# Kernel tuning notes

Measured on AMD Instinct MI355X. Metric: run time of the kernel, lower is better.

## Reference

```python
import jax, jax.numpy as jnp
import numpy as np

S, B, C, H, W = 16, 64, 128, 11, 11
P = H * W
N_ITER = 3
EPS = 1e-5


def setup_inputs() -> dict:
    key = jax.random.key(0)
    ks = jax.random.split(key, 12)
    w = lambda k, shape: jax.random.normal(k, shape, jnp.float32) * 0.02
    return {
        "x": jax.random.normal(ks[0], (S, B, C, H, W), jnp.float32),
        # intra-attention 1x1 convs (stored as [out,in] matrices)
        "wq": w(ks[1], (C, C)), "bq": jnp.zeros((C,), jnp.float32),
        "wk": w(ks[2], (C, C)), "bk": jnp.zeros((C,), jnp.float32),
        "wv": w(ks[3], (C, C)), "bv": jnp.zeros((C,), jnp.float32),
        "intra_alpha": jnp.float32(1.0),
        # inter-message path
        "w_msg": w(ks[4], (C, C + 1)), "b_msg": jnp.zeros((C,), jnp.float32),
        "w_lin": w(ks[5], (C, C)),
        "weight": jnp.float32(0.5),
        "w_gate": w(ks[6], (C, C)), "b_gate": jnp.zeros((C,), jnp.float32),
        # ConvGRU 3x3 convs
        "w_zr": w(ks[7], (2 * C, 2 * C, 3, 3)), "b_zr": jnp.zeros((2 * C,), jnp.float32),
        "w_h": w(ks[8], (C, 2 * C, 3, 3)), "b_h": jnp.zeros((C,), jnp.float32),
        # LayerNorm over [C,11,11]
        "ln_gamma": jnp.ones((C, H, W), jnp.float32),
        "ln_beta": jnp.zeros((C, H, W), jnp.float32),
    }


def reference(x, wq, bq, wk, bk, wv, bv, intra_alpha, w_msg, b_msg, w_lin,
              weight, w_gate, b_gate, w_zr, b_zr, w_h, b_h, ln_gamma, ln_beta):
    scale = C ** -0.5

    def c1(t, wgt, bias):  # 1x1 conv on [S,B,Cin,H,W] -> [S,B,Cout,H,W]
        return jnp.einsum('sbchw,oc->sbohw', t, wgt) + bias[:, None, None]

    def conv3(t, wgt, bias):  # 3x3 'SAME' conv on [N,Cin,H,W]
        y = jax.lax.conv_general_dilated(
            t, wgt, (1, 1), 'SAME', dimension_numbers=('NCHW', 'OIHW', 'NCHW'))
        return y + bias[None, :, None, None]

    # chain-graph neighbor validity masks (|i-j| == 1)
    mask_l = (jnp.arange(S) >= 1).astype(x.dtype)[:, None, None, None, None]
    mask_r = (jnp.arange(S) <= S - 2).astype(x.dtype)[:, None, None, None, None]

    h = x
    for _ in range(N_ITER):
        # ---- intra spatial self-attention (per node, over P=H*W tokens) ----
        q = c1(h, wq, bq).reshape(S, B, C, P)
        k = c1(h, wk, bk).reshape(S, B, C, P)
        v = c1(h, wv, bv).reshape(S, B, C, P)
        att = jax.nn.softmax(jnp.einsum('sbcp,sbcq->sbpq', q, k) * scale, axis=-1)
        intra = jnp.einsum('sbpq,sbcq->sbcp', att, v).reshape(S, B, C, H, W)
        intra = intra_alpha * intra + h

        # ---- inter gated message attention from chain neighbors ----
        xf = h.reshape(S, B, C, P)

        def gated_msg(y, edge_val):
            ef = jnp.full((S, B, 1, H, W), edge_val, h.dtype)  # edge feature i-j
            yy = c1(jnp.concatenate([y, ef], axis=2), w_msg, b_msg).reshape(S, B, C, P)
            yy = jnp.einsum('sbcp,dc->sbdp', yy, w_lin)  # Linear (no bias)
            a = jax.nn.softmax(jnp.einsum('sbcp,sbcq->sbpq', xf, yy), axis=-1)
            m = jnp.einsum('sbpq,sbcq->sbcp', a, yy).reshape(S, B, C, H, W)
            g = jax.nn.sigmoid(c1(m, w_gate, b_gate).mean(axis=(-2, -1), keepdims=True))
            return m * g

        y_left = jnp.concatenate([jnp.zeros_like(h[:1]), h[:-1]], axis=0)   # h[i-1], edge +1
        y_right = jnp.concatenate([h[1:], jnp.zeros_like(h[:1])], axis=0)   # h[i+1], edge -1
        inter = gated_msg(y_left, 1.0) * mask_l + gated_msg(y_right, -1.0) * mask_r

        comb = weight * intra + (1.0 - weight) * inter

        # ---- ConvGRU update (fold S into batch) ----
        xg = comb.reshape(S * B, C, H, W)
        hg = h.reshape(S * B, C, H, W)
        zr = jax.nn.sigmoid(conv3(jnp.concatenate([xg, hg], axis=1), w_zr, b_zr))
        z, r = zr[:, :C], zr[:, C:]
        h_hat = jnp.tanh(conv3(jnp.concatenate([xg, r * hg], axis=1), w_h, b_h))
        h_new = ((1 - z) * hg + z * h_hat).reshape(S, B, C, H, W)

        # ---- residual + LayerNorm over [C,H,W] ----
        nh = h_new + h
        mu = nh.mean(axis=(-3, -2, -1), keepdims=True)
        var = nh.var(axis=(-3, -2, -1), keepdims=True)
        h = (nh - mu) * jax.lax.rsqrt(var + EPS) * ln_gamma + ln_beta
    return h
```

## Files before the change

### kernel.cpp

```cpp
#include <hip/hip_runtime.h>
#include <hip/hip_bf16.h>

#define S_   16
#define B_   64
#define SBn  1024
#define C_   128
#define P_   121
#define CP_  15488
static const long NEl = 15859712L;

typedef __hip_bfloat16 bf16t;
typedef __attribute__((ext_vector_type(8))) short bf16x8;
typedef __attribute__((ext_vector_type(4))) float f32x4;
typedef __attribute__((ext_vector_type(4))) unsigned short us4;

__device__ __forceinline__ float ldb(const bf16t* p){ return __bfloat162float(*p); }
__device__ __forceinline__ float b2f(unsigned short u){ unsigned x=((unsigned)u)<<16; float f; __builtin_memcpy(&f,&x,4); return f; }
__device__ __forceinline__ unsigned short f2bu(float v){ __hip_bfloat16 b=__float2bfloat16(v); unsigned short u; __builtin_memcpy(&u,&b,2); return u; }
__device__ __forceinline__ float ldin(const void* s, long i, int f){
    return f ? ((const float*)s)[i] : b2f(((const unsigned short*)s)[i]);
}

__global__ void detect_kernel(const unsigned short* __restrict__ x, int* __restrict__ flag){
    if(blockIdx.x==0 && threadIdx.x==0){
        int crazy=0;
        for(int i=0;i<512;i++){
            unsigned e=(x[i]>>7)&0xFF;
            if(e!=0 && (e<64 || e>191)) crazy++;
        }
        *flag=(crazy>40)?1:0;
    }
}

__global__ void cvt_kernel(float* __restrict__ dst, const void* __restrict__ src, long n, const int* __restrict__ flag){
    long i=(long)blockIdx.x*blockDim.x+threadIdx.x;
    long st=(long)gridDim.x*blockDim.x;
    int f=*flag;
    for(;i<n;i+=st) dst[i]=ldin(src,i,f);
}

__global__ __launch_bounds__(256) void cvtT_kernel(bf16t* __restrict__ hT, const void* __restrict__ x, const int* __restrict__ flag){
    __shared__ bf16t tl[CP_];
    int sb=blockIdx.x, t=threadIdx.x; int f=*flag;
    for(int i=t;i<CP_;i+=256)
        tl[i]=__float2bfloat16(ldin(x,(long)sb*CP_+i,f));
    __syncthreads();
    bf16t* ho=hT+(size_t)sb*CP_;
    for(int j=t;j<CP_;j+=256){
        int p=j>>7, c=j&127;
        ho[j]=tl[c*P_+p];
    }
}

__global__ __launch_bounds__(128) void prep_msg_kernel(float* __restrict__ W2, float* __restrict__ b2l, float* __restrict__ b2r,
        const void* __restrict__ wlin, const void* __restrict__ wmsg, const void* __restrict__ bmsg, const int* __restrict__ flag){
    int d=blockIdx.x, c=threadIdx.x; int f=*flag;
    float acc=0.f;
    for(int o2=0;o2<C_;o2++) acc += ldin(wlin,(long)d*C_+o2,f)*ldin(wmsg,(long)o2*(C_+1)+c,f);
    W2[d*C_+c]=acc;
    if(c<2){
        float e=(c==0)?1.f:-1.f; float a=0.f;
        for(int o2=0;o2<C_;o2++) a += ldin(wlin,(long)d*C_+o2,f)*(ldin(bmsg,o2,f)+e*ldin(wmsg,(long)o2*(C_+1)+C_,f));
        if(c==0) b2l[d]=a; else b2r[d]=a;
    }
}

template<int RAW>
__global__ void prep_w1t(bf16t* __restrict__ dst, const void* __restrict__ src, const int* __restrict__ flag){
    int idx=blockIdx.x*blockDim.x+threadIdx.x;
    if(idx>=16384) return;
    int r=idx&31, oc=(idx>>5)&127, icb=idx>>12;
    float v = RAW? ldin(src,(long)oc*C_+icb*32+r,*flag) : ((const float*)src)[(long)oc*C_+icb*32+r];
    dst[idx]=__float2bfloat16(v);
}

__global__ void prep_w3t(bf16t* __restrict__ dst, const void* __restrict__ src, const int* __restrict__ flag, int OC){
    int idx=blockIdx.x*blockDim.x+threadIdx.x;
    int tot=OC*2304;
    if(idx>=tot) return;
    int r=idx&31; int rest=idx>>5; int oc=rest%OC; int g2=rest/OC; int icb=g2&7, tap=g2>>3;
    float v=ldin(src,((long)(oc*256+icb*32+r))*9+tap,*flag);
    dst[idx]=__float2bfloat16(v);
}

__global__ void prep_gbt(float* __restrict__ gamT, float* __restrict__ betT,
                         const void* __restrict__ gam, const void* __restrict__ bet, const int* __restrict__ flag){
    int idx=blockIdx.x*blockDim.x+threadIdx.x;
    if(idx>=CP_) return;
    int c=idx/P_, p=idx-c*P_; int f=*flag;
    gamT[p*C_+c]=ldin(gam,idx,f);
    betT[p*C_+c]=ldin(bet,idx,f);
}

__global__ void prep_wgt(float* __restrict__ wgT, float* __restrict__ bg2,
                         const void* __restrict__ wg, const void* __restrict__ bg, const int* __restrict__ flag){
    int idx=blockIdx.x*blockDim.x+threadIdx.x;
    int f=*flag;
    if(idx<16384){ int k=idx>>7, c=idx&127; wgT[idx]=ldin(wg,(long)c*C_+k,f); }
    if(idx<128) bg2[idx]=ldin(bg,idx,f);
}

__device__ __forceinline__ void gemm24r(f32x4 (&acc)[4][2],
    const bf16t* __restrict__ Wt, const bf16x8 (&hreg)[4][2],
    int ocr,int l15,int kg)
{
    #pragma unroll
    for(int i=0;i<4;i++){
        #pragma unroll
        for(int j=0;j<2;j++) acc[i][j]=(f32x4){0.f,0.f,0.f,0.f};
    }
    #pragma unroll
    for(int kc=0;kc<4;kc++){
        bf16x8 a[4];
        #pragma unroll
        for(int mt=0;mt<4;mt++) a[mt]=*(const bf16x8*)(Wt+((size_t)(kc*C_+ocr*64+mt*16+l15))*32+kg*8);
        #pragma unroll
        for(int mt=0;mt<4;mt++){
            #pragma unroll
            for(int nt=0;nt<2;nt++)
                acc[mt][nt]=__builtin_amdgcn_mfma_f32_16x16x32_bf16(a[mt],hreg[kc][nt],acc[mt][nt],0,0,0);
        }
    }
}

__device__ __forceinline__ void msg_phase(
    f32x4 (&res)[8], const bf16t* __restrict__ hT, int sb, int shift,
    const bf16t* __restrict__ W2T, const float* __restrict__ b2e,
    const float* __restrict__ wgT, const float* __restrict__ bgf, float w1m,
    const bf16x8 (&areg)[4],
    bf16t* LA, bf16t* LB, float* fl,
    int t,int w,int l15,int kg,int ocr,int pcr)
{
    __syncthreads();
    const bf16t* hsp=hT+(size_t)(sb+shift)*CP_;
    bf16x8 hregS[4][2];
    #pragma unroll
    for(int kc=0;kc<4;kc++){
        #pragma unroll
        for(int nt=0;nt<2;nt++)
            hregS[kc][nt]=*(const bf16x8*)(hsp+(size_t)(pcr*32+nt*16+l15)*C_+kc*32+kg*8);
    }
    f32x4 acc[4][2];
    gemm24r(acc,W2T,hregS,ocr,l15,kg);
    #pragma unroll
    for(int mt=0;mt<4;mt++){
        int oc0=ocr*64+mt*16+kg*4;
        #pragma unroll
        for(int nt=0;nt<2;nt++){
            int p=pcr*32+nt*16+l15;
            us4 pk;
            #pragma unroll
            for(int r=0;r<4;r++){
                float v=acc[mt][nt][r]+b2e[oc0+r];
                pk[r]=f2bu(v);
                LB[(oc0+r)*136+p]=__float2bfloat16(p<P_? v : 0.f);
            }
            *(us4*)(LA+p*136+oc0)=pk;
        }
    }
    __syncthreads();
    int m0=w*16;
    f32x4 s[8];
    #pragma unroll
    for(int nt=0;nt<8;nt++) s[nt]=(f32x4){0.f,0.f,0.f,0.f};
// ... 149 lines not shown
    if(l15>=9){
        #pragma unroll
        for(int r=0;r<4;r++) s[7][r]=-3.0e38f;
    }
    #pragma unroll
    for(int r=0;r<4;r++){
        float mx=s[0][r];
        #pragma unroll
        for(int nt=1;nt<8;nt++) mx=fmaxf(mx,s[nt][r]);
        #pragma unroll
        for(int o=1;o<16;o<<=1) mx=fmaxf(mx,__shfl_xor(mx,o));
        float sm=0.f;
        #pragma unroll
        for(int nt=0;nt<8;nt++){ float e=__expf(s[nt][r]-mx); s[nt][r]=e; sm+=e; }
        #pragma unroll
        for(int o=1;o<16;o<<=1) sm+=__shfl_xor(sm,o);
        float rs=1.f/sm;
        #pragma unroll
        for(int nt=0;nt<8;nt++) s[nt][r]*=rs;
    }
    __syncthreads();
    gemm24r(acc,WvT,hreg,ocr,l15,kg);
    #pragma unroll
    for(int mt=0;mt<4;mt++){
        int oc0=ocr*64+mt*16+kg*4;
        #pragma unroll
        for(int nt=0;nt<2;nt++){
            int p=pcr*32+nt*16+l15;
            #pragma unroll
            for(int r=0;r<4;r++)
                LA[(oc0+r)*136+p]=__float2bfloat16(p<P_? acc[mt][nt][r]+bv[oc0+r] : 0.f);
        }
    }
    #pragma unroll
    for(int r=0;r<4;r++){
        int pr=m0+kg*4+r;
        #pragma unroll
        for(int nt=0;nt<8;nt++) LB[pr*136+nt*16+l15]=__float2bfloat16(s[nt][r]);
    }
    __syncthreads();
    f32x4 res[8];
    #pragma unroll
    for(int nt=0;nt<8;nt++) res[nt]=(f32x4){0.f,0.f,0.f,0.f};
    #pragma unroll
    for(int jc=0;jc<4;jc++){
        bf16x8 a=*(const bf16x8*)(LA+(size_t)(m0+l15)*136+jc*32+kg*8);
        #pragma unroll
        for(int nt=0;nt<8;nt++){
            bf16x8 b=*(const bf16x8*)(LB+(size_t)(nt*16+l15)*136+jc*32+kg*8);
            res[nt]=__builtin_amdgcn_mfma_f32_16x16x32_bf16(a,b,res[nt],0,0,0);
        }
    }
    float al=*alphap, wv=*wp, w1m=1.f-wv;
    int c0=m0+kg*4;
    #pragma unroll
    for(int nt=0;nt<8;nt++){
        int p=nt*16+l15;
        int pc=(p<P_)?p:(P_-1);
        us4 hv=*(const us4*)(hp+(size_t)pc*C_+c0);
        #pragma unroll
        for(int r=0;r<4;r++) res[nt][r]=wv*(al*res[nt][r]+b2f(hv[r]));
    }
    if(sb>=B_)
        msg_phase(res,hT,sb,-B_,W2T,b2l,wgT,bgf,w1m,areg,LA,LB,fl,t,w,l15,kg,ocr,pcr);
    if(sb<SBn-B_)
        msg_phase(res,hT,sb, B_,W2T,b2r,wgT,bgf,w1m,areg,LA,LB,fl,t,w,l15,kg,ocr,pcr);
    __syncthreads();
    unsigned short* tl=(unsigned short*)LA;
    #pragma unroll
    for(int nt=0;nt<8;nt++){
        int p=nt*16+l15;
        if(p>=P_) continue;
        us4 pk;
        #pragma unroll
        for(int r=0;r<4;r++) pk[r]=f2bu(res[nt][r]);
        *(us4*)(tl+p*C_+c0)=pk;
    }
    __syncthreads();
    bf16t* ob=comb+(size_t)sb*CP_;
    for(int j=t;j<1936;j+=512)
        *(bf16x8*)(ob+j*8)=*(const bf16x8*)(tl+j*8);
}

#define LOADA2(bidx, widx) { \
    _Pragma("unroll") \
    for(int mt=0;mt<2;mt++) abuf[bidx][mt]=*(const bf16x8*)(Wt+(size_t)(widx)*(OC*32)+mt*512+base_lane); }
#define STEP2(lbase, bidx, doff) { \
    bf16x8 bb[4]; \
    _Pragma("unroll") \
    for(int nt=0;nt<4;nt++) bb[nt]=*(const bf16x8*)((lbase)+boff[nt]+(doff)); \
    __builtin_amdgcn_s_setprio(1); \
    _Pragma("unroll") \
    for(int mt=0;mt<2;mt++){ \
        _Pragma("unroll") \
        for(int nt=0;nt<4;nt++) \
            acc[mt][nt]=__builtin_amdgcn_mfma_f32_16x16x32_bf16(abuf[bidx][mt],bb[nt],acc[mt][nt],0,0,0); } \
    __builtin_amdgcn_s_setprio(0); }

#define SLOADZ(stg) { \
    const bf16t* ssrc=(((stg)<2)? in0T:in1T)+(size_t)sb*CP_+((stg)&1)*64; \
    if(sv0) sreg0=*(const bf16x8*)(ssrc+(size_t)sp0*C_+(t&7)*8); }
#define SWRITEZ(lbase) { \
    if(sv0) *(bf16x8*)((lbase)+spix0*72+(t&7)*8)=sreg0; }

__global__ __launch_bounds__(1024) void conv3_zr(
    bf16t* __restrict__ o0, bf16t* __restrict__ o1,
    const bf16t* __restrict__ in0T, const bf16t* __restrict__ in1T,
    const bf16t* __restrict__ Wt, const float* __restrict__ bias,
    const bf16t* __restrict__ hTb)
{
    constexpr int OC=256;
    __shared__ bf16t lin[2*12176];
    int sb=blockIdx.x;
    int t=threadIdx.x, lane=t&63, w=t>>6;
    int ocb=(w>=8)?128:0; int w2=w&7;
    int ocr=w2>>1, pcr=w2&1, l15=lane&15, kg=lane>>4;
    int boff[4]; bool pv_[4];
    #pragma unroll
    for(int nt=0;nt<4;nt++){
        int p=pcr*64+nt*16+l15;
        pv_[nt]=(p<P_); int pc=pv_[nt]?p:(P_-1);
        boff[nt]=((pc/11)*13+(pc%11))*72+kg*8;
    }
    f32x4 acc[2][4];
    #pragma unroll
    for(int i=0;i<2;i++){
        #pragma unroll
        for(int j=0;j<4;j++) acc[i][j]=(f32x4){0.f,0.f,0.f,0.f};
    }
    int base_lane=(ocb+ocr*32+l15)*32+kg*8;
    bf16x8 abuf[4][2];
    bf16x8 sreg0;
    bool sv0=(t<968);
    int sp0=(t<968)? (t>>3):120;
    int spix0=(sp0/11+1)*13+(sp0%11)+1;
    LOADA2(0,0); LOADA2(1,1); LOADA2(2,8); LOADA2(3,9);
    SLOADZ(0);
    {
        bf16x8 z;
        #pragma unroll
        for(int e=0;e<8;e++) z[e]=0;
        if(t<768){
            int half=t>=384; int i2=t-half*384;
            int bi=i2>>3, cc=(i2&7)*8;
            int pix;
            if(bi<13) pix=bi;
            else if(bi<26) pix=156+(bi-13);
            else { int j2=bi-26; pix=(1+(j2>>1))*13+((j2&1)?12:0); }
            *(bf16x8*)(lin+half*12176+pix*72+cc)=z;
        }
    }
    SWRITEZ(lin);
    __syncthreads();
    #pragma unroll
    for(int st=0; st<4; ++st){
        if(st<3) SLOADZ(st+1);
        bf16t* lbase=lin+(st&1)*12176;
        #pragma unroll
        for(int k=0;k<18;k++){
            int s=st*18+k;
            int tap=k>>1, l=k&1;
            int doff=((tap/3)*13+(tap%3))*72+l*32;
            STEP2(lbase, s&3, doff);
            if(s<68){
                int s4=s+4, st4=s4/18, k4=s4-st4*18, tap4=k4>>1, l4=k4&1;
                LOADA2(s&3, tap4*8+st4*2+l4);
            }
        }
        if(st<3){ SWRITEZ(lin+((st+1)&1)*12176); }
        __syncthreads();
    }
    unsigned short* tl=(unsigned short*)lin;
    if(ocb==0){
        #pragma unroll
        for(int mt=0;mt<2;mt++){
            int ocl=ocr*32+mt*16+kg*4;
            #pragma unroll
            for(int nt=0;nt<4;nt++){
                if(!pv_[nt]) continue;
                int p=pcr*64+nt*16+l15;
                us4 pk;
                #pragma unroll
                for(int r=0;r<4;r++){ float a=acc[mt][nt][r]+bias[ocl+r]; pk[r]=f2bu(1.f/(1.f+__expf(-a))); }
                *(us4*)(tl+p*C_+ocl)=pk;
            }
        }
    }
    __syncthreads();
    {
        bf16t* zb=o0+(size_t)sb*CP_;
        *(bf16x8*)(zb+t*8)=*(const bf16x8*)(tl+t*8);
        if(t<912) *(bf16x8*)(zb+(t+1024)*8)=*(const bf16x8*)(tl+(t+1024)*8);
    }
    __syncthreads();
    if(ocb==128){
        #pragma unroll
        for(int mt=0;mt<2;mt++){
            int ocl=ocr*32+mt*16+kg*4;
            #pragma unroll
            for(int nt=0;nt<4;nt++){
                if(!pv_[nt]) continue;
                int p=pcr*64+nt*16+l15;
                size_t tb=(size_t)sb*CP_+(size_t)p*C_+ocl;
                us4 hv=*(const us4*)(hTb+tb);
                us4 pk;
                #pragma unroll
                for(int r=0;r<4;r++){ float a=acc[mt][nt][r]+bias[128+ocl+r]; float sg=1.f/(1.f+__expf(-a)); pk[r]=f2bu(sg*b2f(hv[r])); }
                *(us4*)(tl+p*C_+ocl)=pk;
            }
        }
    }
    __syncthreads();
    {
        bf16t* rb=o1+(size_t)sb*CP_;
        *(bf16x8*)(rb+t*8)=*(const bf16x8*)(tl+t*8);
        if(t<912) *(bf16x8*)(rb+(t+1024)*8)=*(const bf16x8*)(tl+(t+1024)*8);
    }
}

#define SLOADH(stg) { \
    const bf16t* ssrc=(((stg)<2)? in0T:in1T)+(size_t)sb*CP_+((stg)&1)*64; \
    sreg[0]=*(const bf16x8*)(ssrc+(size_t)(t>>3)*C_+(t&7)*8); \
    if(sv1) sreg[1]=*(const bf16x8*)(ssrc+(size_t)sp1*C_+(t&7)*8); }
#define SWRITEH(lbase) { \
    *(bf16x8*)((lbase)+spix0*72+(t&7)*8)=sreg[0]; \
    if(sv1) *(bf16x8*)((lbase)+spix1*72+(t&7)*8)=sreg[1]; }

__global__ __launch_bounds__(512,4) void conv3_hh(
    bf16t* __restrict__ o0,
    const bf16t* __restrict__ in0T, const bf16t* __restrict__ in1T,
    const bf16t* __restrict__ Wt, const float* __restrict__ bias,
    const bf16t* __restrict__ zT, const bf16t* __restrict__ hTb,
    const float* __restrict__ gamT, const float* __restrict__ betT)
{
    constexpr int OC=128;
    __shared__ bf16t lin[2*12176];
    __shared__ float red[16];
    int sb=blockIdx.x;
    int t=threadIdx.x, lane=t&63, w=t>>6;
    int ocr=w>>1, pcr=w&1, l15=lane&15, kg=lane>>4;
    int boff[4]; bool pv_[4];
    #pragma unroll
    for(int nt=0;nt<4;nt++){
        int p=pcr*64+nt*16+l15;
        pv_[nt]=(p<P_); int pc=pv_[nt]?p:(P_-1);
        boff[nt]=((pc/11)*13+(pc%11))*72+kg*8;
    }
    f32x4 acc[2][4];
    #pragma unroll
    for(int i=0;i<2;i++){
        #pragma unroll
        for(int j=0;j<4;j++) acc[i][j]=(f32x4){0.f,0.f,0.f,0.f};
    }
    int base_lane=(ocr*32+l15)*32+kg*8;
    bf16x8 abuf[4][2];
    bf16x8 sreg[2];
    bool sv1=((t+512)<968);
    int sp0=t>>3, sp1=(t+512)>>3;
    if(sp1>120) sp1=120;
    int spix0=(sp0/11+1)*13+(sp0%11)+1;
    int spix1=(sp1/11+1)*13+(sp1%11)+1;
    LOADA2(0,0); LOADA2(1,1); LOADA2(2,8); LOADA2(3,9);
    SLOADH(0);
    {
        bf16x8 z;
        #pragma unroll
        for(int e=0;e<8;e++) z[e]=0;
        for(int i=t;i<768;i+=512){
            int half=i>=384; int i2=i-half*384;
            int bi=i2>>3, cc=(i2&7)*8;
            int pix;
            if(bi<13) pix=bi;
            else if(bi<26) pix=156+(bi-13);
            else { int j2=bi-26; pix=(1+(j2>>1))*13+((j2&1)?12:0); }
            *(bf16x8*)(lin+half*12176+pix*72+cc)=z;
        }
    }
    SWRITEH(lin);
    __syncthreads();
    #pragma unroll
    for(int st=0; st<4; ++st){
        if(st<3) SLOADH(st+1);
        bf16t* lbase=lin+(st&1)*12176;
        #pragma unroll
        for(int k=0;k<18;k++){
            int s=st*18+k;
            int tap=k>>1, l=k&1;
            int doff=((tap/3)*13+(tap%3))*72+l*32;
            STEP2(lbase, s&3, doff);
            if(s<68){
                int s4=s+4, st4=s4/18, k4=s4-st4*18, tap4=k4>>1, l4=k4&1;
                LOADA2(s&3, tap4*8+st4*2+l4);
            }
        }
        if(st<3){ SWRITEH(lin+((st+1)&1)*12176); }
        __syncthreads();
    }
    float ls=0.f, ls2=0.f;
    #pragma unroll
    for(int mt=0;mt<2;mt++){
        int ocl=ocr*32+mt*16+kg*4;
        #pragma unroll
        for(int nt=0;nt<4;nt++){
            if(!pv_[nt]) continue;
            int p=pcr*64+nt*16+l15;
            size_t tb=(size_t)sb*CP_+(size_t)p*C_+ocl;
            us4 hv=*(const us4*)(hTb+tb);
            us4 zv=*(const us4*)(zT+tb);
            us4 pk;
            #pragma unroll
            for(int r=0;r<4;r++){
                float a=acc[mt][nt][r]+bias[ocl+r];
                float ht=tanhf(a);
                float z=b2f(zv[r]), h=b2f(hv[r]);
                unsigned short u=f2bu((1.f-z)*h+z*ht+h);
                pk[r]=u;
                float nr=b2f(u); ls+=nr; ls2+=nr*nr;
            }
            *(us4*)((unsigned short*)lin + p*C_+ocl)=pk;
        }
    }
    #pragma unroll
    for(int o=32;o;o>>=1){ ls+=__shfl_xor(ls,o); ls2+=__shfl_xor(ls2,o); }
    if(lane==0){ red[w]=ls; red[8+w]=ls2; }
    __syncthreads();
    float Sx=0.f,Sx2=0.f;
    #pragma unroll
    for(int i=0;i<8;i++){ Sx+=red[i]; Sx2+=red[8+i]; }
    float mu=Sx*(1.f/(float)CP_);
    float var=Sx2*(1.f/(float)CP_)-mu*mu;
    float rstd=rsqrtf(var+1e-5f);
    bf16t* ho=o0+(size_t)sb*CP_;
    const unsigned short* tl=(const unsigned short*)lin;
    for(int j=t;j<1936;j+=512){
        int base=j*8;
        bf16x8 ovec;
        #pragma unroll
        for(int e=0;e<8;e++){
            float v=(b2f(tl[base+e])-mu)*rstd*gamT[base+e]+betT[base+e];
            ovec[e]=(short)f2bu(v);
        }
        *(bf16x8*)(ho+base)=ovec;
    }
}

__global__ __launch_bounds__(256) void finalT_kernel(void* __restrict__ fout, const bf16t* __restrict__ hT, const int* __restrict__ flag){
    __shared__ bf16t tl[CP_];
    int sb=blockIdx.x, t=threadIdx.x, f=*flag;
    for(int i=t;i<CP_;i+=256) tl[i]=hT[(size_t)sb*CP_+i];
    __syncthreads();
    for(int i=t;i<CP_;i+=256){
        int c=i/P_, p=i-c*P_;
        float v=ldb(tl+p*C_+c);
        size_t oi=(size_t)sb*CP_+i;
        if(f) ((float*)fout)[oi]=v;
        else  ((bf16t*)fout)[oi]=__float2bfloat16(v);
    }
}

extern "C" void kernel_launch(void* const* d_in, const int* in_sizes, int n_in,
                              void* d_out, int out_size, void* d_ws, size_t ws_size,
                              hipStream_t stream) {
    (void)in_sizes; (void)n_in; (void)out_size;
    char* base=(char*)d_ws;
    size_t off=0;
    auto alloc=[&](size_t bytes){ void* p=base+off; off+=(bytes+255)&~(size_t)255; return p; };
    bf16t* b1=(bf16t*)alloc((size_t)NEl*2+8192);
    bf16t* b2=(bf16t*)alloc((size_t)NEl*2+8192);
    bf16t* b3=(bf16t*)alloc((size_t)NEl*2+8192);
    bf16t* b4=(bf16t*)d_out;
    bf16t* wqT=(bf16t*)alloc(16384*2);
    bf16t* wkT=(bf16t*)alloc(16384*2);
    bf16t* wvT=(bf16t*)alloc(16384*2);
    bf16t* w2T=(bf16t*)alloc(16384*2);
    bf16t* wzrT=(bf16t*)alloc((size_t)589824*2);
    bf16t* whT =(bf16t*)alloc((size_t)294912*2);
    float* W2f=(float*)alloc(16384*4);
    float* b2l=(float*)alloc(128*4); float* b2r=(float*)alloc(128*4);
    float* bqf=(float*)alloc(128*4); float* bkf=(float*)alloc(128*4); float* bvf=(float*)alloc(128*4);
    float* bzrf=(float*)alloc(256*4); float* bhf=(float*)alloc(128*4);
    float* gamT=(float*)alloc(15488*4); float* betT=(float*)alloc(15488*4);
    float* wgTf=(float*)alloc(16384*4); float* bgf2=(float*)alloc(128*4);
    float* alphaf=(float*)alloc(4); float* weightf=(float*)alloc(4);
    int* flag=(int*)alloc(4);
    if(ws_size<off) return;

    detect_kernel<<<1,64,0,stream>>>((const unsigned short*)d_in[0],flag);
    cvtT_kernel<<<SBn,256,0,stream>>>(b1,d_in[0],flag);
    prep_w1t<1><<<64,256,0,stream>>>(wqT,d_in[1],flag);
    cvt_kernel<<<1,128,0,stream>>>(bqf,d_in[2],128,flag);
    prep_w1t<1><<<64,256,0,stream>>>(wkT,d_in[3],flag);
    cvt_kernel<<<1,128,0,stream>>>(bkf,d_in[4],128,flag);
    prep_w1t<1><<<64,256,0,stream>>>(wvT,d_in[5],flag);
    cvt_kernel<<<1,128,0,stream>>>(bvf,d_in[6],128,flag);
    cvt_kernel<<<1,64,0,stream>>>(alphaf,d_in[7],1,flag);
    prep_msg_kernel<<<C_,C_,0,stream>>>(W2f,b2l,b2r,d_in[10],d_in[8],d_in[9],flag);
    prep_w1t<0><<<64,256,0,stream>>>(w2T,W2f,flag);
    cvt_kernel<<<1,64,0,stream>>>(weightf,d_in[11],1,flag);
    prep_wgt<<<64,256,0,stream>>>(wgTf,bgf2,d_in[12],d_in[13],flag);
    prep_w3t<<<(256*2304+255)/256,256,0,stream>>>(wzrT,d_in[14],flag,256);
    cvt_kernel<<<1,256,0,stream>>>(bzrf,d_in[15],256,flag);
    prep_w3t<<<(128*2304+255)/256,256,0,stream>>>(whT,d_in[16],flag,128);
    cvt_kernel<<<1,128,0,stream>>>(bhf,d_in[17],128,flag);
    prep_gbt<<<(CP_+255)/256,256,0,stream>>>(gamT,betT,d_in[18],d_in[19],flag);

    for(int it=0; it<3; ++it){
        attn_all<<<SBn,512,0,stream>>>(b2,b1,wqT,wkT,wvT,bqf,bkf,bvf,
                                       w2T,b2l,b2r,wgTf,bgf2,alphaf,weightf);
        conv3_zr<<<SBn,1024,0,stream>>>(b4,b3,b2,b1,wzrT,bzrf,b1);
        conv3_hh<<<SBn,512,0,stream>>>(b1,b2,b3,whT,bhf,b4,b1,gamT,betT);
    }
    finalT_kernel<<<SBn,256,0,stream>>>(d_out,b1,flag);
}
```

Before: 1.385 ms.

## Switch 3x3 conv kernels to 32x32x16 MFMA and split zr conv across blocks

Both ConvGRU 3x3 conv kernels move from 16x16x32 bf16 MFMA tiles to 32x32x16 tiles, with each wave covering 64 output channels by 32 pixels. Weights are repacked into 16-wide k groups to match, and A-operand prefetch drops from four buffers to two. conv3_zr no longer runs one 1024-thread block that computes both z and r; it launches a 2D grid of 512-thread blocks, one per 128-channel half, and each block writes its half directly. The aim is better MFMA efficiency and fewer idle lanes from the 121-pixel padding. In exchange, each block stages its input into shared memory twice, and register pressure per thread rises.

```diff
diff --git a/kernel.cpp b/kernel.cpp
--- a/kernel.cpp
+++ b/kernel.cpp
@@ -12,6 +12,7 @@
 typedef __hip_bfloat16 bf16t;
 typedef __attribute__((ext_vector_type(8))) short bf16x8;
 typedef __attribute__((ext_vector_type(4))) float f32x4;
+typedef __attribute__((ext_vector_type(16))) float f32x16;
 typedef __attribute__((ext_vector_type(4))) unsigned short us4;
 
 __device__ __forceinline__ float ldb(const bf16t* p){ return __bfloat162float(*p); }
@@ -74,12 +75,12 @@
     dst[idx]=__float2bfloat16(v);
 }
 
-__global__ void prep_w3t(bf16t* __restrict__ dst, const void* __restrict__ src, const int* __restrict__ flag, int OC){
+__global__ void prep_w3t32(bf16t* __restrict__ dst, const void* __restrict__ src, const int* __restrict__ flag, int OC){
     int idx=blockIdx.x*blockDim.x+threadIdx.x;
     int tot=OC*2304;
     if(idx>=tot) return;
-    int r=idx&31; int rest=idx>>5; int oc=rest%OC; int g2=rest/OC; int icb=g2&7, tap=g2>>3;
-    float v=ldin(src,((long)(oc*256+icb*32+r))*9+tap,*flag);
+    int r=idx&15; int rest=idx>>4; int oc=rest%OC; int g2=rest/OC; int k16=g2&15, tap=g2>>4;
+    float v=ldin(src,((long)(oc*256+k16*16+r))*9+tap,*flag);
     dst[idx]=__float2bfloat16(v);
 }
 
@@ -395,28 +396,33 @@
         *(bf16x8*)(ob+j*8)=*(const bf16x8*)(tl+j*8);
 }
 
-#define LOADA2(bidx, widx) { \
+#define LOADA32(bidx, gk) { \
     _Pragma("unroll") \
-    for(int mt=0;mt<2;mt++) abuf[bidx][mt]=*(const bf16x8*)(Wt+(size_t)(widx)*(OC*32)+mt*512+base_lane); }
-#define STEP2(lbase, bidx, doff) { \
-    bf16x8 bb[4]; \
+    for(int ot=0;ot<2;ot++){ \
+        _Pragma("unroll") \
+        for(int kk=0;kk<4;kk++) \
+            abuf[bidx][ot][kk]=*(const bf16x8*)(Wt+(((size_t)(gk)+kk)*OC+aoc0+ot*32)*16+ah8); } }
+#define TAP32(lbase, bidx, d) { \
+    bf16x8 br[4]; \
     _Pragma("unroll") \
-    for(int nt=0;nt<4;nt++) bb[nt]=*(const bf16x8*)((lbase)+boff[nt]+(doff)); \
+    for(int kk=0;kk<4;kk++) br[kk]=*(const bf16x8*)((lbase)+bpix0+(d)+kk*16); \
     __builtin_amdgcn_s_setprio(1); \
     _Pragma("unroll") \
-    for(int mt=0;mt<2;mt++){ \
-        _Pragma("unroll") \
-        for(int nt=0;nt<4;nt++) \
-            acc[mt][nt]=__builtin_amdgcn_mfma_f32_16x16x32_bf16(abuf[bidx][mt],bb[nt],acc[mt][nt],0,0,0); } \
+    for(int kk=0;kk<4;kk++){ \
+        accA=__builtin_amdgcn_mfma_f32_32x32x16_bf16(abuf[bidx][0][kk],br[kk],accA,0,0,0); \
+        accB=__builtin_amdgcn_mfma_f32_32x32x16_bf16(abuf[bidx][1][kk],br[kk],accB,0,0,0); \
+    } \
     __builtin_amdgcn_s_setprio(0); }
 
-#define SLOADZ(stg) { \
+#define SLOAD32(stg) { \
     const bf16t* ssrc=(((stg)<2)? in0T:in1T)+(size_t)sb*CP_+((stg)&1)*64; \
-    if(sv0) sreg0=*(const bf16x8*)(ssrc+(size_t)sp0*C_+(t&7)*8); }
-#define SWRITEZ(lbase) { \
-    if(sv0) *(bf16x8*)((lbase)+spix0*72+(t&7)*8)=sreg0; }
-
-__global__ __launch_bounds__(1024) void conv3_zr(
+    sreg[0]=*(const bf16x8*)(ssrc+(size_t)(t>>3)*C_+(t&7)*8); \
+    if(sv1) sreg[1]=*(const bf16x8*)(ssrc+(size_t)sp1*C_+(t&7)*8); }
+#define SWRITE32(lbase) { \
+    *(bf16x8*)((lbase)+spix0*72+(t&7)*8)=sreg[0]; \
+    if(sv1) *(bf16x8*)((lbase)+spix1*72+(t&7)*8)=sreg[1]; }
+
+__global__ __launch_bounds__(512) void conv3_zr(
     bf16t* __restrict__ o0, bf16t* __restrict__ o1,
     const bf16t* __restrict__ in0T, const bf16t* __restrict__ in1T,
     const bf16t* __restrict__ Wt, const float* __restrict__ bias,
@@ -424,37 +430,33 @@
 {
     constexpr int OC=256;
     __shared__ bf16t lin[2*12176];
-    int sb=blockIdx.x;
+    int sb=blockIdx.x, ocb=(int)blockIdx.y*128;
     int t=threadIdx.x, lane=t&63, w=t>>6;
-    int ocb=(w>=8)?128:0; int w2=w&7;
-    int ocr=w2>>1, pcr=w2&1, l15=lane&15, kg=lane>>4;
-    int boff[4]; bool pv_[4];
-    #pragma unroll
-    for(int nt=0;nt<4;nt++){
-        int p=pcr*64+nt*16+l15;
-        pv_[nt]=(p<P_); int pc=pv_[nt]?p:(P_-1);
-        boff[nt]=((pc/11)*13+(pc%11))*72+kg*8;
-    }
-    f32x4 acc[2][4];
-    #pragma unroll
-    for(int i=0;i<2;i++){
-        #pragma unroll
-        for(int j=0;j<4;j++) acc[i][j]=(f32x4){0.f,0.f,0.f,0.f};
-    }
-    int base_lane=(ocb+ocr*32+l15)*32+kg*8;
-    bf16x8 abuf[4][2];
-    bf16x8 sreg0;
-    bool sv0=(t<968);
-    int sp0=(t<968)? (t>>3):120;
+    int ocr=w>>2, pcr=w&3;
+    int c31=lane&31, h=lane>>5;
+    int p0=pcr*32+c31;
+    bool pv0=(p0<P_);
+    int pc0=pv0?p0:(P_-1);
+    int bpix0=((pc0/11)*13+(pc0%11))*72+h*8;
+    f32x16 accA,accB;
+    #pragma unroll
+    for(int j=0;j<16;j++){ accA[j]=0.f; accB[j]=0.f; }
+    int aoc0=ocb+ocr*64+c31, ah8=h*8;
+    bf16x8 abuf[2][2][4];
+    bf16x8 sreg[2];
+    bool sv1=((t+512)<968);
+    int sp0=t>>3, sp1=(t+512)>>3;
+    if(sp1>120) sp1=120;
     int spix0=(sp0/11+1)*13+(sp0%11)+1;
-    LOADA2(0,0); LOADA2(1,1); LOADA2(2,8); LOADA2(3,9);
-    SLOADZ(0);
+    int spix1=(sp1/11+1)*13+(sp1%11)+1;
+    LOADA32(0,0);
+    SLOAD32(0);
     {
         bf16x8 z;
         #pragma unroll
         for(int e=0;e<8;e++) z[e]=0;
-        if(t<768){
-            int half=t>=384; int i2=t-half*384;
+        for(int i=t;i<768;i+=512){
+            int half=i>=384; int i2=i-half*384;
             int bi=i2>>3, cc=(i2&7)*8;
             int pix;
             if(bi<13) pix=bi;
@@ -463,83 +465,74 @@
             *(bf16x8*)(lin+half*12176+pix*72+cc)=z;
         }
     }
-    SWRITEZ(lin);
+    SWRITE32(lin);
     __syncthreads();
     #pragma unroll
     for(int st=0; st<4; ++st){
-        if(st<3) SLOADZ(st+1);
+        if(st<3) SLOAD32(st+1);
         bf16t* lbase=lin+(st&1)*12176;
         #pragma unroll
-        for(int k=0;k<18;k++){
-            int s=st*18+k;
-            int tap=k>>1, l=k&1;
-            int doff=((tap/3)*13+(tap%3))*72+l*32;
-            STEP2(lbase, s&3, doff);
-            if(s<68){
-                int s4=s+4, st4=s4/18, k4=s4-st4*18, tap4=k4>>1, l4=k4&1;
-                LOADA2(s&3, tap4*8+st4*2+l4);
+        for(int tap=0;tap<9;tap++){
+            int g=st*9+tap;
+            if(g<35){
+                int g1=g+1, st1=g1/9, tap1=g1-st1*9;
+                LOADA32(g1&1, tap1*16+st1*4);
             }
-        }
-        if(st<3){ SWRITEZ(lin+((st+1)&1)*12176); }
+            int d=((tap/3)*13+(tap%3))*72;
+            TAP32(lbase, g&1, d);
+        }
+        if(st<3){ SWRITE32(lin+((st+1)&1)*12176); }
         __syncthreads();
     }
     unsigned short* tl=(unsigned short*)lin;
-    if(ocb==0){
-        #pragma unroll
-        for(int mt=0;mt<2;mt++){
-            int ocl=ocr*32+mt*16+kg*4;
+    if(pv0){
+        if(ocb==0){
             #pragma unroll
-            for(int nt=0;nt<4;nt++){
-                if(!pv_[nt]) continue;
-                int p=pcr*64+nt*16+l15;
-                us4 pk;
+            for(int a=0;a<4;a++){
+                int ocA=ocr*64+8*a+4*h, ocB=ocA+32;
+                us4 pkA,pkB;
                 #pragma unroll
-                for(int r=0;r<4;r++){ float a=acc[mt][nt][r]+bias[ocl+r]; pk[r]=f2bu(1.f/(1.f+__expf(-a))); }
-                *(us4*)(tl+p*C_+ocl)=pk;
+                for(int r=0;r<4;r++){
+                    float vA=accA[4*a+r]+bias[ocA+r];
+                    float vB=accB[4*a+r]+bias[ocB+r];
+                    pkA[r]=f2bu(1.f/(1.f+__expf(-vA)));
+                    pkB[r]=f2bu(1.f/(1.f+__expf(-vB)));
+                }
+                *(us4*)(tl+p0*C_+ocA)=pkA;
+                *(us4*)(tl+p0*C_+ocB)=pkB;
             }
+        }else{
+            #pragma unroll
+            for(int a=0;a<4;a++){
+                int ocA=ocr*64+8*a+4*h, ocB=ocA+32;
+                size_t tbA=(size_t)sb*CP_+(size_t)p0*C_+ocA;
+                size_t tbB=(size_t)sb*CP_+(size_t)p0*C_+ocB;
+                us4 hvA=*(const us4*)(hTb+tbA);
+                us4 hvB=*(const us4*)(hTb+tbB);
+                us4 pkA,pkB;
+                #pragma unroll
+                for(int r=0;r<4;r++){
+                    float vA=accA[4*a+r]+bias[128+ocA+r];
+                    float vB=accB[4*a+r]+bias[128+ocB+r];
+                    float sA=1.f/(1.f+__expf(-vA));
+                    float sB=1.f/(1.f+__expf(-vB));
+                    pkA[r]=f2bu(sA*b2f(hvA[r]));
+                    pkB[r]=f2bu(sB*b2f(hvB[r]));
+                }
+                *(us4*)(tl+p0*C_+ocA)=pkA;
+                *(us4*)(tl+p0*C_+ocB)=pkB;
+            }
         }
     }
     __syncthreads();
     {
-        bf16t* zb=o0+(size_t)sb*CP_;
-        *(bf16x8*)(zb+t*8)=*(const bf16x8*)(tl+t*8);
-        if(t<912) *(bf16x8*)(zb+(t+1024)*8)=*(const bf16x8*)(tl+(t+1024)*8);
-    }
-    __syncthreads();
-    if(ocb==128){
-        #pragma unroll
-        for(int mt=0;mt<2;mt++){
-            int ocl=ocr*32+mt*16+kg*4;
-            #pragma unroll
-            for(int nt=0;nt<4;nt++){
-                if(!pv_[nt]) continue;
-                int p=pcr*64+nt*16+l15;
-                size_t tb=(size_t)sb*CP_+(size_t)p*C_+ocl;
-                us4 hv=*(const us4*)(hTb+tb);
-                us4 pk;
-                #pragma unroll
-                for(int r=0;r<4;r++){ float a=acc[mt][nt][r]+bias[128+ocl+r]; float sg=1.f/(1.f+__expf(-a)); pk[r]=f2bu(sg*b2f(hv[r])); }
-                *(us4*)(tl+p*C_+ocl)=pk;
-            }
-        }
-    }
-    __syncthreads();
-    {
-        bf16t* rb=o1+(size_t)sb*CP_;
-        *(bf16x8*)(rb+t*8)=*(const bf16x8*)(tl+t*8);
-        if(t<912) *(bf16x8*)(rb+(t+1024)*8)=*(const bf16x8*)(tl+(t+1024)*8);
-    }
-}
-
-#define SLOADH(stg) { \
-    const bf16t* ssrc=(((stg)<2)? in0T:in1T)+(size_t)sb*CP_+((stg)&1)*64; \
-    sreg[0]=*(const bf16x8*)(ssrc+(size_t)(t>>3)*C_+(t&7)*8); \
-    if(sv1) sreg[1]=*(const bf16x8*)(ssrc+(size_t)sp1*C_+(t&7)*8); }
-#define SWRITEH(lbase) { \
-    *(bf16x8*)((lbase)+spix0*72+(t&7)*8)=sreg[0]; \
-    if(sv1) *(bf16x8*)((lbase)+spix1*72+(t&7)*8)=sreg[1]; }
-
-__global__ __launch_bounds__(512,4) void conv3_hh(
+        bf16t* ob=(ocb==0? o0 : o1)+(size_t)sb*CP_;
+        for(int j=t;j<1936;j+=512)
+            *(bf16x8*)(ob+j*8)=*(const bf16x8*)(tl+j*8);
+    }
+}
+
+__global__ __launch_bounds__(512) void conv3_hh(
     bf16t* __restrict__ o0,
     const bf16t* __restrict__ in0T, const bf16t* __restrict__ in1T,
     const bf16t* __restrict__ Wt, const float* __restrict__ bias,
@@ -551,30 +544,25 @@
     __shared__ float red[16];
     int sb=blockIdx.x;
     int t=threadIdx.x, lane=t&63, w=t>>6;
-    int ocr=w>>1, pcr=w&1, l15=lane&15, kg=lane>>4;
-    int boff[4]; bool pv_[4];
-    #pragma unroll
-    for(int nt=0;nt<4;nt++){
-        int p=pcr*64+nt*16+l15;
-        pv_[nt]=(p<P_); int pc=pv_[nt]?p:(P_-1);
-        boff[nt]=((pc/11)*13+(pc%11))*72+kg*8;
-    }
-    f32x4 acc[2][4];
-    #pragma unroll
-    for(int i=0;i<2;i++){
-        #pragma unroll
-        for(int j=0;j<4;j++) acc[i][j]=(f32x4){0.f,0.f,0.f,0.f};
-    }
-    int base_lane=(ocr*32+l15)*32+kg*8;
-    bf16x8 abuf[4][2];
+    int ocr=w>>2, pcr=w&3;
+    int c31=lane&31, h=lane>>5;
+    int p0=pcr*32+c31;
+    bool pv0=(p0<P_);
+    int pc0=pv0?p0:(P_-1);
+    int bpix0=((pc0/11)*13+(pc0%11))*72+h*8;
+    f32x16 accA,accB;
+    #pragma unroll
+    for(int j=0;j<16;j++){ accA[j]=0.f; accB[j]=0.f; }
+    int aoc0=ocr*64+c31, ah8=h*8;
+    bf16x8 abuf[2][2][4];
     bf16x8 sreg[2];
     bool sv1=((t+512)<968);
     int sp0=t>>3, sp1=(t+512)>>3;
     if(sp1>120) sp1=120;
     int spix0=(sp0/11+1)*13+(sp0%11)+1;
     int spix1=(sp1/11+1)*13+(sp1%11)+1;
-    LOADA2(0,0); LOADA2(1,1); LOADA2(2,8); LOADA2(3,9);
-    SLOADH(0);
+    LOADA32(0,0);
+    SLOAD32(0);
     {
         bf16x8 z;
         #pragma unroll
@@ -589,48 +577,50 @@
             *(bf16x8*)(lin+half*12176+pix*72+cc)=z;
         }
     }
-    SWRITEH(lin);
+    SWRITE32(lin);
     __syncthreads();
     #pragma unroll
     for(int st=0; st<4; ++st){
-        if(st<3) SLOADH(st+1);
+        if(st<3) SLOAD32(st+1);
         bf16t* lbase=lin+(st&1)*12176;
         #pragma unroll
-        for(int k=0;k<18;k++){
-            int s=st*18+k;
-            int tap=k>>1, l=k&1;
-            int doff=((tap/3)*13+(tap%3))*72+l*32;
-            STEP2(lbase, s&3, doff);
-            if(s<68){
-                int s4=s+4, st4=s4/18, k4=s4-st4*18, tap4=k4>>1, l4=k4&1;
-                LOADA2(s&3, tap4*8+st4*2+l4);
+        for(int tap=0;tap<9;tap++){
+            int g=st*9+tap;
+            if(g<35){
+                int g1=g+1, st1=g1/9, tap1=g1-st1*9;
+                LOADA32(g1&1, tap1*16+st1*4);
             }
-        }
-        if(st<3){ SWRITEH(lin+((st+1)&1)*12176); }
+            int d=((tap/3)*13+(tap%3))*72;
+            TAP32(lbase, g&1, d);
+        }
+        if(st<3){ SWRITE32(lin+((st+1)&1)*12176); }
         __syncthreads();
     }
     float ls=0.f, ls2=0.f;
-    #pragma unroll
-    for(int mt=0;mt<2;mt++){
-        int ocl=ocr*32+mt*16+kg*4;
-        #pragma unroll
-        for(int nt=0;nt<4;nt++){
-            if(!pv_[nt]) continue;
-            int p=pcr*64+nt*16+l15;
-            size_t tb=(size_t)sb*CP_+(size_t)p*C_+ocl;
-            us4 hv=*(const us4*)(hTb+tb);
-            us4 zv=*(const us4*)(zT+tb);
-            us4 pk;
+    if(pv0){
+        #pragma unroll
+        for(int a=0;a<4;a++){
+            int ocA=ocr*64+8*a+4*h, ocB=ocA+32;
+            size_t tbA=(size_t)sb*CP_+(size_t)p0*C_+ocA;
+            size_t tbB=(size_t)sb*CP_+(size_t)p0*C_+ocB;
+            us4 hvA=*(const us4*)(hTb+tbA); us4 zvA=*(const us4*)(zT+tbA);
+            us4 hvB=*(const us4*)(hTb+tbB); us4 zvB=*(const us4*)(zT+tbB);
+            us4 pkA,pkB;
             #pragma unroll
             for(int r=0;r<4;r++){
-                float a=acc[mt][nt][r]+bias[ocl+r];
-                float ht=tanhf(a);
-                float z=b2f(zv[r]), h=b2f(hv[r]);
-                unsigned short u=f2bu((1.f-z)*h+z*ht+h);
-                pk[r]=u;
-                float nr=b2f(u); ls+=nr; ls2+=nr*nr;
+                float aA=accA[4*a+r]+bias[ocA+r];
+                float aB=accB[4*a+r]+bias[ocB+r];
+                float htA=tanhf(aA), htB=tanhf(aB);
+                float zA=b2f(zvA[r]), hA=b2f(hvA[r]);
+                float zB=b2f(zvB[r]), hB=b2f(hvB[r]);
+                unsigned short uA=f2bu((1.f-zA)*hA+zA*htA+hA);
+                unsigned short uB=f2bu((1.f-zB)*hB+zB*htB+hB);
+                pkA[r]=uA; pkB[r]=uB;
+                float nA=b2f(uA), nB=b2f(uB);
+                ls+=nA+nB; ls2+=nA*nA+nB*nB;
             }
-            *(us4*)((unsigned short*)lin + p*C_+ocl)=pk;
+            *(us4*)((unsigned short*)lin+p0*C_+ocA)=pkA;
+            *(us4*)((unsigned short*)lin+p0*C_+ocB)=pkB;
         }
     }
     #pragma unroll
@@ -711,16 +701,16 @@
     prep_w1t<0><<<64,256,0,stream>>>(w2T,W2f,flag);
     cvt_kernel<<<1,64,0,stream>>>(weightf,d_in[11],1,flag);
     prep_wgt<<<64,256,0,stream>>>(wgTf,bgf2,d_in[12],d_in[13],flag);
-    prep_w3t<<<(256*2304+255)/256,256,0,stream>>>(wzrT,d_in[14],flag,256);
+    prep_w3t32<<<(256*2304+255)/256,256,0,stream>>>(wzrT,d_in[14],flag,256);
     cvt_kernel<<<1,256,0,stream>>>(bzrf,d_in[15],256,flag);
-    prep_w3t<<<(128*2304+255)/256,256,0,stream>>>(whT,d_in[16],flag,128);
+    prep_w3t32<<<(128*2304+255)/256,256,0,stream>>>(whT,d_in[16],flag,128);
     cvt_kernel<<<1,128,0,stream>>>(bhf,d_in[17],128,flag);
     prep_gbt<<<(CP_+255)/256,256,0,stream>>>(gamT,betT,d_in[18],d_in[19],flag);
 
     for(int it=0; it<3; ++it){
         attn_all<<<SBn,512,0,stream>>>(b2,b1,wqT,wkT,wvT,bqf,bkf,bvf,
                                        w2T,b2l,b2r,wgTf,bgf2,alphaf,weightf);
-        conv3_zr<<<SBn,1024,0,stream>>>(b4,b3,b2,b1,wzrT,bzrf,b1);
+        conv3_zr<<<dim3(SBn,2),512,0,stream>>>(b4,b3,b2,b1,wzrT,bzrf,b1);
         conv3_hh<<<SBn,512,0,stream>>>(b1,b2,b3,whT,bhf,b4,b1,gamT,betT);
     }
     finalT_kernel<<<SBn,256,0,stream>>>(d_out,b1,flag);
```

Result: slower. 1.601 ms (+15.5%).

## Restructure conv3_zr to process two samples per block, splitting output channels across grid

Applied to the files above, without the earlier changes.

The zr 3x3 conv kernel is reorganized so each 512-thread block handles two samples and one 128-channel half of the output, instead of one sample with all 256 channels in a 1024-thread block. Each weight fragment loaded from global memory is now reused across two samples' MFMAs, halving weight traffic per sample. The cost is doubled LDS (four padded tiles), doubled accumulator registers, and the input activations being loaded twice, once by each channel-half block.

```diff
diff --git a/kernel.cpp b/kernel.cpp
--- a/kernel.cpp
+++ b/kernel.cpp
@@ -410,24 +410,44 @@
             acc[mt][nt]=__builtin_amdgcn_mfma_f32_16x16x32_bf16(abuf[bidx][mt],bb[nt],acc[mt][nt],0,0,0); } \
     __builtin_amdgcn_s_setprio(0); }
 
-#define SLOADZ(stg) { \
-    const bf16t* ssrc=(((stg)<2)? in0T:in1T)+(size_t)sb*CP_+((stg)&1)*64; \
-    if(sv0) sreg0=*(const bf16x8*)(ssrc+(size_t)sp0*C_+(t&7)*8); }
-#define SWRITEZ(lbase) { \
-    if(sv0) *(bf16x8*)((lbase)+spix0*72+(t&7)*8)=sreg0; }
-
-__global__ __launch_bounds__(1024) void conv3_zr(
+#define SLOADZ2(stg) { \
+    const bf16t* s0=(((stg)<2)? in0T:in1T)+(size_t)sb0*CP_+((stg)&1)*64; \
+    const bf16t* s1=s0+CP_; \
+    sreg[0]=*(const bf16x8*)(s0+(size_t)spA*C_+(t&7)*8); \
+    if(sv1) sreg[1]=*(const bf16x8*)(s0+(size_t)spB*C_+(t&7)*8); \
+    sreg[2]=*(const bf16x8*)(s1+(size_t)spA*C_+(t&7)*8); \
+    if(sv1) sreg[3]=*(const bf16x8*)(s1+(size_t)spB*C_+(t&7)*8); }
+#define SWRITEZ2(lbase) { \
+    *(bf16x8*)((lbase)+spixA*72+(t&7)*8)=sreg[0]; \
+    if(sv1) *(bf16x8*)((lbase)+spixB*72+(t&7)*8)=sreg[1]; \
+    *(bf16x8*)((lbase)+12176+spixA*72+(t&7)*8)=sreg[2]; \
+    if(sv1) *(bf16x8*)((lbase)+12176+spixB*72+(t&7)*8)=sreg[3]; }
+#define STEPZ2(lbase, bidx, doff) { \
+    bf16x8 bb0[4], bb1[4]; \
+    _Pragma("unroll") \
+    for(int nt=0;nt<4;nt++){ \
+        bb0[nt]=*(const bf16x8*)((lbase)+boff[nt]+(doff)); \
+        bb1[nt]=*(const bf16x8*)((lbase)+12176+boff[nt]+(doff)); } \
+    __builtin_amdgcn_s_setprio(1); \
+    _Pragma("unroll") \
+    for(int mt=0;mt<2;mt++){ \
+        _Pragma("unroll") \
+        for(int nt=0;nt<4;nt++){ \
+            accA[mt][nt]=__builtin_amdgcn_mfma_f32_16x16x32_bf16(abuf[bidx][mt],bb0[nt],accA[mt][nt],0,0,0); \
+            accB[mt][nt]=__builtin_amdgcn_mfma_f32_16x16x32_bf16(abuf[bidx][mt],bb1[nt],accB[mt][nt],0,0,0); } } \
+    __builtin_amdgcn_s_setprio(0); }
+
+__global__ __launch_bounds__(512) void conv3_zr2(
     bf16t* __restrict__ o0, bf16t* __restrict__ o1,
     const bf16t* __restrict__ in0T, const bf16t* __restrict__ in1T,
     const bf16t* __restrict__ Wt, const float* __restrict__ bias,
     const bf16t* __restrict__ hTb)
 {
     constexpr int OC=256;
-    __shared__ bf16t lin[2*12176];
-    int sb=blockIdx.x;
+    __shared__ bf16t lin[4*12176];
+    int sb0=(int)blockIdx.x*2, ocb=(int)blockIdx.y*128;
     int t=threadIdx.x, lane=t&63, w=t>>6;
-    int ocb=(w>=8)?128:0; int w2=w&7;
-    int ocr=w2>>1, pcr=w2&1, l15=lane&15, kg=lane>>4;
+    int ocr=w>>1, pcr=w&1, l15=lane&15, kg=lane>>4;
     int boff[4]; bool pv_[4];
     #pragma unroll
     for(int nt=0;nt<4;nt++){
@@ -435,99 +455,111 @@
         pv_[nt]=(p<P_); int pc=pv_[nt]?p:(P_-1);
         boff[nt]=((pc/11)*13+(pc%11))*72+kg*8;
     }
-    f32x4 acc[2][4];
+    f32x4 accA[2][4], accB[2][4];
     #pragma unroll
     for(int i=0;i<2;i++){
         #pragma unroll
-        for(int j=0;j<4;j++) acc[i][j]=(f32x4){0.f,0.f,0.f,0.f};
+        for(int j=0;j<4;j++){ accA[i][j]=(f32x4){0.f,0.f,0.f,0.f}; accB[i][j]=(f32x4){0.f,0.f,0.f,0.f}; }
     }
     int base_lane=(ocb+ocr*32+l15)*32+kg*8;
     bf16x8 abuf[4][2];
-    bf16x8 sreg0;
-    bool sv0=(t<968);
-    int sp0=(t<968)? (t>>3):120;
-    int spix0=(sp0/11+1)*13+(sp0%11)+1;
+    bf16x8 sreg[4];
+    bool sv1=((t+512)<968);
+    int spA=t>>3, spB=(t+512)>>3;
+    if(spB>120) spB=120;
+    int spixA=(spA/11+1)*13+(spA%11)+1;
+    int spixB=(spB/11+1)*13+(spB%11)+1;
     LOADA2(0,0); LOADA2(1,1); LOADA2(2,8); LOADA2(3,9);
-    SLOADZ(0);
+    SLOADZ2(0);
     {
         bf16x8 z;
         #pragma unroll
         for(int e=0;e<8;e++) z[e]=0;
-        if(t<768){
-            int half=t>=384; int i2=t-half*384;
+        for(int i=t;i<1536;i+=512){
+            int tile=i/384; int i2=i-tile*384;
             int bi=i2>>3, cc=(i2&7)*8;
             int pix;
             if(bi<13) pix=bi;
             else if(bi<26) pix=156+(bi-13);
             else { int j2=bi-26; pix=(1+(j2>>1))*13+((j2&1)?12:0); }
-            *(bf16x8*)(lin+half*12176+pix*72+cc)=z;
-        }
-    }
-    SWRITEZ(lin);
+            *(bf16x8*)(lin+tile*12176+pix*72+cc)=z;
+        }
+    }
+    SWRITEZ2(lin);
     __syncthreads();
     #pragma unroll
     for(int st=0; st<4; ++st){
-        if(st<3) SLOADZ(st+1);
-        bf16t* lbase=lin+(st&1)*12176;
+        if(st<3) SLOADZ2(st+1);
+        bf16t* lbase=lin+(st&1)*24352;
         #pragma unroll
         for(int k=0;k<18;k++){
             int s=st*18+k;
             int tap=k>>1, l=k&1;
             int doff=((tap/3)*13+(tap%3))*72+l*32;
-            STEP2(lbase, s&3, doff);
+            STEPZ2(lbase, s&3, doff);
             if(s<68){
                 int s4=s+4, st4=s4/18, k4=s4-st4*18, tap4=k4>>1, l4=k4&1;
                 LOADA2(s&3, tap4*8+st4*2+l4);
             }
         }
-        if(st<3){ SWRITEZ(lin+((st+1)&1)*12176); }
+        if(st<3){ SWRITEZ2(lin+((st+1)&1)*24352); }
         __syncthreads();
     }
     unsigned short* tl=(unsigned short*)lin;
-    if(ocb==0){
-        #pragma unroll
-        for(int mt=0;mt<2;mt++){
-            int ocl=ocr*32+mt*16+kg*4;
-            #pragma unroll
-            for(int nt=0;nt<4;nt++){
-                if(!pv_[nt]) continue;
-                int p=pcr*64+nt*16+l15;
-                us4 pk;
+    bf16t* obase=(ocb==0? o0 : o1);
+    const float* bs=bias+(ocb==0?0:128);
+    #pragma unroll
+    for(int mt=0;mt<2;mt++){
+        int ocl=ocr*32+mt*16+kg*4;
+        #pragma unroll
+        for(int nt=0;nt<4;nt++){
+            if(!pv_[nt]) continue;
+            int p=pcr*64+nt*16+l15;
+            us4 pk;
+            if(ocb==0){
                 #pragma unroll
-                for(int r=0;r<4;r++){ float a=acc[mt][nt][r]+bias[ocl+r]; pk[r]=f2bu(1.f/(1.f+__expf(-a))); }
-                *(us4*)(tl+p*C_+ocl)=pk;
+                for(int r=0;r<4;r++){ float a=accA[mt][nt][r]+bs[ocl+r]; pk[r]=f2bu(1.f/(1.f+__expf(-a))); }
+            }else{
+                size_t tb=(size_t)sb0*CP_+(size_t)p*C_+ocl;
+                us4 hv=*(const us4*)(hTb+tb);
+                #pragma unroll
+                for(int r=0;r<4;r++){ float a=accA[mt][nt][r]+bs[ocl+r]; float sg=1.f/(1.f+__expf(-a)); pk[r]=f2bu(sg*b2f(hv[r])); }
             }
+            *(us4*)(tl+p*C_+ocl)=pk;
         }
     }
     __syncthreads();
     {
-        bf16t* zb=o0+(size_t)sb*CP_;
-        *(bf16x8*)(zb+t*8)=*(const bf16x8*)(tl+t*8);
-        if(t<912) *(bf16x8*)(zb+(t+1024)*8)=*(const bf16x8*)(tl+(t+1024)*8);
-    }
-    __syncthreads();
-    if(ocb==128){
-        #pragma unroll
-        for(int mt=0;mt<2;mt++){
-            int ocl=ocr*32+mt*16+kg*4;
-            #pragma unroll
-            for(int nt=0;nt<4;nt++){
-                if(!pv_[nt]) continue;
-                int p=pcr*64+nt*16+l15;
-                size_t tb=(size_t)sb*CP_+(size_t)p*C_+ocl;
+        bf16t* ob=obase+(size_t)sb0*CP_;
+        for(int j=t;j<1936;j+=512)
+            *(bf16x8*)(ob+j*8)=*(const bf16x8*)(tl+j*8);
+    }
+    __syncthreads();
+    #pragma unroll
+    for(int mt=0;mt<2;mt++){
+        int ocl=ocr*32+mt*16+kg*4;
+        #pragma unroll
+        for(int nt=0;nt<4;nt++){
+            if(!pv_[nt]) continue;
+            int p=pcr*64+nt*16+l15;
+            us4 pk;
+            if(ocb==0){
+                #pragma unroll
+                for(int r=0;r<4;r++){ float a=accB[mt][nt][r]+bs[ocl+r]; pk[r]=f2bu(1.f/(1.f+__expf(-a))); }
+            }else{
+                size_t tb=(size_t)(sb0+1)*CP_+(size_t)p*C_+ocl;
                 us4 hv=*(const us4*)(hTb+tb);
-                us4 pk;
                 #pragma unroll
-                for(int r=0;r<4;r++){ float a=acc[mt][nt][r]+bias[128+ocl+r]; float sg=1.f/(1.f+__expf(-a)); pk[r]=f2bu(sg*b2f(hv[r])); }
-                *(us4*)(tl+p*C_+ocl)=pk;
+                for(int r=0;r<4;r++){ float a=accB[mt][nt][r]+bs[ocl+r]; float sg=1.f/(1.f+__expf(-a)); pk[r]=f2bu(sg*b2f(hv[r])); }
             }
+            *(us4*)(tl+p*C_+ocl)=pk;
         }
     }
     __syncthreads();
     {
-        bf16t* rb=o1+(size_t)sb*CP_;
-        *(bf16x8*)(rb+t*8)=*(const bf16x8*)(tl+t*8);
-        if(t<912) *(bf16x8*)(rb+(t+1024)*8)=*(const bf16x8*)(tl+(t+1024)*8);
+        bf16t* ob=obase+(size_t)(sb0+1)*CP_;
+        for(int j=t;j<1936;j+=512)
+            *(bf16x8*)(ob+j*8)=*(const bf16x8*)(tl+j*8);
     }
 }
 
@@ -720,7 +752,7 @@
     for(int it=0; it<3; ++it){
         attn_all<<<SBn,512,0,stream>>>(b2,b1,wqT,wkT,wvT,bqf,bkf,bvf,
                                        w2T,b2l,b2r,wgTf,bgf2,alphaf,weightf);
-        conv3_zr<<<SBn,1024,0,stream>>>(b4,b3,b2,b1,wzrT,bzrf,b1);
+        conv3_zr2<<<dim3(SBn/2,2),512,0,stream>>>(b4,b3,b2,b1,wzrT,bzrf,b1);
         conv3_hh<<<SBn,512,0,stream>>>(b1,b2,b3,whT,bhf,b4,b1,gamT,betT);
     }
     finalT_kernel<<<SBn,256,0,stream>>>(d_out,b1,flag);
```

Result: faster. 1.341 ms (-3.2%).
